# Optimization experiments

Hardware: AMD Instinct MI355X
Metric: run time of the kernel (lower is better)

Reference implementation:

```python
import jax, jax.numpy as jnp
import numpy as np

EPS = 1e-6
DECAY = 0.99
COMMIT = 0.25           # CONFIG['commitment_cost']
GRAPH_BIAS_SCALE = 0.8  # CONFIG['graph_bias_scale']
CONTEXT_INFLUENCE = 0.5 # CONFIG['context_influence']

N, LATENT, K = 16384, 512, 8192


def setup_inputs() -> dict:
    key = jax.random.key(0)
    ks = jax.random.split(key, 9)
    z_real = jax.random.normal(ks[0], (N, LATENT), jnp.float32)
    z_imag = jax.random.normal(ks[1], (N, LATENT), jnp.float32)
    ctx_real = jax.random.normal(ks[2], (N, LATENT), jnp.float32)
    ctx_imag = jax.random.normal(ks[3], (N, LATENT), jnp.float32)
    prev_symbol_idx = jax.random.randint(ks[4], (N,), 0, K, jnp.int32)
    codebook = jax.random.normal(ks[5], (K, 2 * LATENT), jnp.float32)
    adjacency = jax.random.normal(ks[6], (K, K), jnp.float32)
    # nn.Linear-style init scale for the context gate
    gate_w = jax.random.normal(ks[7], (K, 2 * LATENT), jnp.float32) / np.sqrt(2 * LATENT)
    gate_b = jax.random.normal(ks[8], (K,), jnp.float32) / np.sqrt(2 * LATENT)
    cluster_size = jnp.zeros((K,), jnp.float32)
    embed_avg = codebook.copy()
    return dict(z_real=z_real, z_imag=z_imag, ctx_real=ctx_real, ctx_imag=ctx_imag,
                prev_symbol_idx=prev_symbol_idx, codebook=codebook, adjacency=adjacency,
                gate_w=gate_w, gate_b=gate_b, cluster_size=cluster_size, embed_avg=embed_avg)


def reference(z_real, z_imag, ctx_real, ctx_imag, prev_symbol_idx, codebook,
              adjacency, gate_w, gate_b, cluster_size, embed_avg):
    n_symbols = codebook.shape[0]
    z_flat = jnp.concatenate([z_real, z_imag], axis=-1)          # [N, 2D]
    # squared euclidean distances to codebook: [N, K]
    d = (jnp.sum(z_flat ** 2, axis=1, keepdims=True)
         + jnp.sum(codebook ** 2, axis=1)
         - 2.0 * z_flat @ codebook.T)
    # graph-context bias
    static_prior = adjacency[prev_symbol_idx]                    # [N, K] row gather
    ctx_flat = jnp.concatenate([ctx_real, ctx_imag], axis=-1)    # [N, 2D]
    context_bias = ctx_flat @ gate_w.T + gate_b                  # [N, K]
    combined_prior = jax.nn.sigmoid(static_prior) * (1.0 + CONTEXT_INFLUENCE * jnp.tanh(context_bias))
    d = d - GRAPH_BIAS_SCALE * combined_prior

    min_indices = jnp.argmin(d, axis=1)                          # [N]
    z_q = codebook[min_indices]                                  # [N, 2D]

    # training-mode EMA codebook update (one-hot matmuls == segment sums)
    counts = jax.ops.segment_sum(jnp.ones_like(min_indices, jnp.float32), min_indices,
                                 num_segments=n_symbols)
    embed_sum = jax.ops.segment_sum(z_flat, min_indices, num_segments=n_symbols)
    new_cluster_size = cluster_size * DECAY + (1.0 - DECAY) * counts
    new_embed_avg = embed_avg * DECAY + (1.0 - DECAY) * embed_sum
    n_total = jnp.sum(new_cluster_size)
    cs = (new_cluster_size + EPS) / (n_total + n_symbols * EPS) * n_total
    new_codebook = new_embed_avg / cs[:, None]

    loss_vq = jnp.mean((z_q - jax.lax.stop_gradient(z_flat)) ** 2)
    loss_commit = jnp.mean((jax.lax.stop_gradient(z_q) - z_flat) ** 2)
    loss = loss_vq + COMMIT * loss_commit

    # straight-through estimator; complex output represented as concat(real, imag)
    z_q_st = z_flat + jax.lax.stop_gradient(z_q - z_flat)        # [N, 2D]
    return z_q_st, loss, min_indices, new_codebook, new_cluster_size, new_embed_avg
```

## Files before the change

### kernel.cpp

```cpp
#include <hip/hip_runtime.h>
#include <hip/hip_bf16.h>


#define NR 16384
#define DH 512
#define D2 1024
#define KS 8192
#define BK 128
#define BN 128
#define KC 64
#define KSPLIT 4
#define KRANGE (KS / KSPLIT)
#define NKT (KRANGE / BK)
#define TILE_B 16384

typedef __bf16 bf16x8 __attribute__((ext_vector_type(8)));
typedef float f32x4 __attribute__((ext_vector_type(4)));

#define WS_CNORM 0
#define WS_LOSS  32768
#define WS_NTOT  32776
#define WS_CAND  33024
#define WS_WIDX  (33024 + NR * 64 * 8)

typedef const __attribute__((address_space(1))) void* gas_t;
typedef __attribute__((address_space(3))) void* las_t;
__device__ __forceinline__ void gld16(const void* g, void* l) {
  __builtin_amdgcn_global_load_lds((gas_t)g, (las_t)l, 16, 0, 0);
}

#define LDSF(t, row, sl)                                                     \
  (*(const bf16x8*)((const char*)sbuf + (t)*TILE_B + (row)*128 +             \
                    (((sl) ^ ((row) & 7)) * 16)))

__global__ __launch_bounds__(256) void k_cvt(
    const float* __restrict__ zr, const float* __restrict__ zi,
    const float* __restrict__ cr, const float* __restrict__ ci,
    const float* __restrict__ cb, const float* __restrict__ gw,
    __hip_bfloat16* __restrict__ zb, __hip_bfloat16* __restrict__ xb,
    __hip_bfloat16* __restrict__ cbb, __hip_bfloat16* __restrict__ gwb) {
  const int flat = blockIdx.x * 256 + threadIdx.x;
  const int r_all = flat >> 7;
  const int g = flat & 127;
  const float* s0;
  const float* s1;
  __hip_bfloat16* dst;
  int r;
  if (r_all < NR)                { r = r_all;              s0 = zr; s1 = zi;      dst = zb;  }
  else if (r_all < 2 * NR)       { r = r_all - NR;         s0 = cr; s1 = ci;      dst = xb;  }
  else if (r_all < 2 * NR + KS)  { r = r_all - 2 * NR;     s0 = cb; s1 = nullptr; dst = cbb; }
  else                           { r = r_all - 2 * NR - KS; s0 = gw; s1 = nullptr; dst = gwb; }
  const int c = g * 8;
  const float* src;
  if (s1) src = (c < DH) ? s0 + (size_t)r * DH + c : s1 + (size_t)r * DH + (c - DH);
  else    src = s0 + (size_t)r * D2 + c;
  f32x4 f0 = *(const f32x4*)src;
  f32x4 f1 = *(const f32x4*)(src + 4);
  bf16x8 h;
  h[0] = (__bf16)f0.x; h[1] = (__bf16)f0.y; h[2] = (__bf16)f0.z; h[3] = (__bf16)f0.w;
  h[4] = (__bf16)f1.x; h[5] = (__bf16)f1.y; h[6] = (__bf16)f1.z; h[7] = (__bf16)f1.w;
  const int chunk = g >> 3, sl = g & 7;
  const int rr = r & 127, rb = r >> 7;
  const int slS = sl ^ (rr & 7);
  const size_t off = ((size_t)(rb * 16 + chunk) * 128 + rr) * 64 + slS * 8;
  *(bf16x8*)(dst + off) = h;
}

__global__ __launch_bounds__(64) void k_cnorm(const float* __restrict__ cb,
                                              float* __restrict__ cnorm) {
  int k = blockIdx.x, lane = threadIdx.x;
  const float* row = cb + (size_t)k * D2;
  float acc = 0.f;
#pragma unroll
  for (int j = 0; j < 4; ++j) {
    f32x4 v = *(const f32x4*)(row + j * 256 + lane * 4);
    acc += v.x * v.x + v.y * v.y + v.z * v.z + v.w * v.w;
  }
#pragma unroll
  for (int off = 32; off; off >>= 1) acc += __shfl_xor(acc, off);
  if (lane == 0) cnorm[k] = acc;
}

__global__ __launch_bounds__(256, 2) void k_phase1(
    const int* __restrict__ prev,
    const __hip_bfloat16* __restrict__ zb, const __hip_bfloat16* __restrict__ xb,
    const __hip_bfloat16* __restrict__ cbb, const __hip_bfloat16* __restrict__ gwb,
    const float* __restrict__ adj, const float* __restrict__ gb,
    const float* __restrict__ cnorm, int2* __restrict__ cand) {
  __shared__ unsigned short sbuf[4 * BK * KC];

  const int tid = threadIdx.x;
  const int lane = tid & 63;
  const int wid = tid >> 6;
  const int wavek = wid >> 1;
  const int waven = wid & 1;
  const int r16 = lane & 15;
  const int quad = lane >> 4;
  const int nb = blockIdx.x;
  const int n0 = nb * BN;
  const int bk = blockIdx.y;

  int nout[4];
  const float* arow[4];
#pragma unroll
  for (int nf = 0; nf < 4; ++nf) {
    nout[nf] = n0 + waven * 64 + nf * 16 + r16;
    arow[nf] = adj + (size_t)prev[nout[nf]] * KS;
  }

  float v0[4], v1[4];
  int i0[4], i1[4];
#pragma unroll
  for (int nf = 0; nf < 4; ++nf) { v0[nf] = 3.4e38f; v1[nf] = 3.4e38f; i0[nf] = 0; i1[nf] = 0; }

  for (int kt = 0; kt < NKT; ++kt) {
    const int ktg = bk * NKT + kt;
    const int k0 = ktg * BK;
    f32x4 accS[4][4], accX[4][4];
#pragma unroll
    for (int a = 0; a < 4; ++a)
#pragma unroll
      for (int b = 0; b < 4; ++b) {
        accS[a][b] = (f32x4){0.f, 0.f, 0.f, 0.f};
        accX[a][b] = (f32x4){0.f, 0.f, 0.f, 0.f};
      }

    for (int c = 0; c < D2 / KC; ++c) {
      const char* tb0 = (const char*)zb  + ((size_t)nb * 16 + c) * TILE_B;
      const char* tb1 = (const char*)xb  + ((size_t)nb * 16 + c) * TILE_B;
      const char* tb2 = (const char*)cbb + ((size_t)ktg * 16 + c) * TILE_B;
      const char* tb3 = (const char*)gwb + ((size_t)ktg * 16 + c) * TILE_B;
#pragma unroll
      for (int i = 0; i < 4; ++i) {
        const int o = (wid * 4 + i) * 1024;
        const int so = o + lane * 16;
        gld16(tb0 + so, (char*)sbuf + 0 * TILE_B + o);
        gld16(tb1 + so, (char*)sbuf + 1 * TILE_B + o);
        gld16(tb2 + so, (char*)sbuf + 2 * TILE_B + o);
        gld16(tb3 + so, (char*)sbuf + 3 * TILE_B + o);
      }
      __syncthreads();

#pragma unroll
      for (int s = 0; s < 2; ++s) {
        const int sl = s * 4 + quad;
        {
          bf16x8 a[4], b[4];
#pragma unroll
          for (int kf = 0; kf < 4; ++kf) a[kf] = LDSF(2, wavek * 64 + kf * 16 + r16, sl);
#pragma unroll
          for (int nf = 0; nf < 4; ++nf) b[nf] = LDSF(0, waven * 64 + nf * 16 + r16, sl);
#pragma unroll
          for (int kf = 0; kf < 4; ++kf)
#pragma unroll
            for (int nf = 0; nf < 4; ++nf)
              accS[kf][nf] =
                  __builtin_amdgcn_mfma_f32_16x16x32_bf16(a[kf], b[nf], accS[kf][nf], 0, 0, 0);
        }
        {
          bf16x8 a[4], b[4];
#pragma unroll
          for (int kf = 0; kf < 4; ++kf) a[kf] = LDSF(3, wavek * 64 + kf * 16 + r16, sl);
#pragma unroll
          for (int nf = 0; nf < 4; ++nf) b[nf] = LDSF(1, waven * 64 + nf * 16 + r16, sl);
#pragma unroll
          for (int kf = 0; kf < 4; ++kf)
#pragma unroll
            for (int nf = 0; nf < 4; ++nf)
              accX[kf][nf] =
                  __builtin_amdgcn_mfma_f32_16x16x32_bf16(a[kf], b[nf], accX[kf][nf], 0, 0, 0);
        }
      }
      __syncthreads();
    }

#pragma unroll
    for (int kf = 0; kf < 4; ++kf) {
      const int kb = k0 + wavek * 64 + kf * 16 + quad * 4;
      const f32x4 cn = *(const f32x4*)(cnorm + kb);
      const f32x4 g4 = *(const f32x4*)(gb + kb);
#pragma unroll
      for (int nf = 0; nf < 4; ++nf) {
        const f32x4 a4 = *(const f32x4*)(arow[nf] + kb);
#pragma unroll
        for (int r = 0; r < 4; ++r) {
          float s = accS[kf][nf][r];
          float x = accX[kf][nf][r] + g4[r];
          float sig = __fdividef(1.f, 1.f + __expf(-a4[r]));
          float e2 = __expf(2.f * x);
          float th = 1.f - __fdividef(2.f, e2 + 1.f);
          float sc = cn[r] - 2.f * s - 0.8f * sig * (1.f + 0.5f * th);
          int kk = kb + r;
          if (sc < v1[nf]) {
            if (sc < v0[nf]) {
              v1[nf] = v0[nf]; i1[nf] = i0[nf];
              v0[nf] = sc;     i0[nf] = kk;
            } else {
              v1[nf] = sc; i1[nf] = kk;
            }
          }
        }
      }
    }
  }

#pragma unroll
  for (int nf = 0; nf < 4; ++nf) {
    const int n = nout[nf];
    const int slot = ((bk * 2 + wavek) * 4 + quad) * 2;
    int2* p = cand + (size_t)n * 64 + slot;
    p[0] = make_int2(__float_as_int(v0[nf]), i0[nf]);
    p[1] = make_int2(__float_as_int(v1[nf]), i1[nf]);
  }
}

__global__ __launch_bounds__(256) void k_rescore(
    const float* __restrict__ zr, const float* __restrict__ zi,
    const float* __restrict__ cr, const float* __restrict__ ci,
    const int* __restrict__ prev, const float* __restrict__ cb,
    const float* __restrict__ adj, const float* __restrict__ gw,
    const float* __restrict__ gb, const int2* __restrict__ cand,
    int* __restrict__ widx, float* __restrict__ out_idx) {
  const int n = blockIdx.x * 4 + (threadIdx.x >> 6);
  const int lane = threadIdx.x & 63;

  f32x4 zv[4], xv[4];
#pragma unroll
  for (int j = 0; j < 4; ++j) {
    const int col = j * 256 + lane * 4;
    zv[j] = (col < DH) ? *(const f32x4*)(zr + (size_t)n * DH + col)
                       : *(const f32x4*)(zi + (size_t)n * DH + col - DH);
    xv[j] = (col < DH) ? *(const f32x4*)(cr + (size_t)n * DH + col)
                       : *(const f32x4*)(ci + (size_t)n * DH + col - DH);
  }

  int2 e = cand[(size_t)n * 64 + lane];
  float asc = __int_as_float(e.x);
  int aid = e.y;
  float m = asc;
#pragma unroll
  for (int off = 32; off; off >>= 1) m = fminf(m, __shfl_xor(m, off));
  unsigned long long mask = __ballot(asc <= m + 1.5f);

  const float* arow = adj + (size_t)prev[n] * KS;
  float best = 3.4e38f;
  int bid = 1 << 30;
  while (mask) {
    const int b = __ffsll((unsigned long long)mask) - 1;
    mask &= mask - 1;
    const int cidx = __shfl(aid, b);
    const float* crow = cb + (size_t)cidx * D2;
    const float* grow = gw + (size_t)cidx * D2;
    float sd = 0.f, xd = 0.f, cn = 0.f;
#pragma unroll
    for (int j = 0; j < 4; ++j) {
      f32x4 c4 = *(const f32x4*)(crow + j * 256 + lane * 4);
      f32x4 g4 = *(const f32x4*)(grow + j * 256 + lane * 4);
      sd += zv[j].x * c4.x + zv[j].y * c4.y + zv[j].z * c4.z + zv[j].w * c4.w;
      cn += c4.x * c4.x + c4.y * c4.y + c4.z * c4.z + c4.w * c4.w;
      xd += xv[j].x * g4.x + xv[j].y * g4.y + xv[j].z * g4.z + xv[j].w * g4.w;
    }
#pragma unroll
    for (int off = 32; off; off >>= 1) {
      sd += __shfl_xor(sd, off);
      cn += __shfl_xor(cn, off);
      xd += __shfl_xor(xd, off);
    }
    float xb2 = xd + gb[cidx];
    float sig = 1.f / (1.f + expf(-arow[cidx]));
    float th = tanhf(xb2);
    float sc = cn - 2.f * sd - 0.8f * sig * (1.f + 0.5f * th);
    if (sc < best || (sc == best && cidx < bid)) { best = sc; bid = cidx; }
  }
  if (lane == 0) { widx[n] = bid; out_idx[n] = (float)bid; }
}

__global__ __launch_bounds__(256) void k_gather(
    const float* __restrict__ zr, const float* __restrict__ zi,
    const float* __restrict__ cb, const int* __restrict__ widx,
    float* __restrict__ out0, float* __restrict__ esum, float* __restrict__ cnt,
    double* __restrict__ loss) {
  __shared__ float red[4];
  const int n = blockIdx.x, tid = threadIdx.x;
  const int w = widx[n];
  const int e = tid * 4;
  f32x4 zv = (e < DH) ? *(const f32x4*)(zr + (size_t)n * DH + e)
                      : *(const f32x4*)(zi + (size_t)n * DH + e - DH);
  f32x4 cq = *(const f32x4*)(cb + (size_t)w * D2 + e);
  f32x4 d, o;
  d.x = cq.x - zv.x; d.y = cq.y - zv.y; d.z = cq.z - zv.z; d.w = cq.w - zv.w;
  o.x = zv.x + d.x;  o.y = zv.y + d.y;  o.z = zv.z + d.z;  o.w = zv.w + d.w;
  *(f32x4*)(out0 + (size_t)n * D2 + e) = o;
  atomicAdd(esum + (size_t)w * D2 + e + 0, zv.x);
  atomicAdd(esum + (size_t)w * D2 + e + 1, zv.y);
  atomicAdd(esum + (size_t)w * D2 + e + 2, zv.z);
  atomicAdd(esum + (size_t)w * D2 + e + 3, zv.w);
  float lp = d.x * d.x + d.y * d.y + d.z * d.z + d.w * d.w;
#pragma unroll
  for (int off = 32; off; off >>= 1) lp += __shfl_xor(lp, off);
  if ((tid & 63) == 0) red[tid >> 6] = lp;
  __syncthreads();
  if (tid == 0) {
    atomicAdd(loss, (double)(red[0] + red[1] + red[2] + red[3]));
    atomicAdd(cnt + w, 1.0f);
  }
}

__global__ __launch_bounds__(256) void k_cs(const float* __restrict__ cs_in,
                                            float* __restrict__ o4,
                                            float* __restrict__ ntot,
                                            const double* __restrict__ loss,
                                            float* __restrict__ o1) {
  __shared__ float red[4];
  const int k = blockIdx.x * 256 + threadIdx.x;
  const float c = o4[k];
  const float ncs = cs_in[k] * 0.99f + 0.01f * c;
  o4[k] = ncs;
  float lp = ncs;
#pragma unroll
  for (int off = 32; off; off >>= 1) lp += __shfl_xor(lp, off);
  if ((threadIdx.x & 63) == 0) red[threadIdx.x >> 6] = lp;
  __syncthreads();
  if (threadIdx.x == 0) atomicAdd(ntot, red[0] + red[1] + red[2] + red[3]);
  if (blockIdx.x == 0 && threadIdx.x == 0)
    o1[0] = (float)(1.25 * loss[0] / 16777216.0);
}

__global__ __launch_bounds__(256) void k_final(const float* __restrict__ eavg,
                                               const float* __restrict__ o4,
                                               const float* __restrict__ ntotp,
                                               float* __restrict__ o3,
                                               float* __restrict__ o5) {
  const int k = blockIdx.x, tid = threadIdx.x;
  const float ntot = *ntotp;
  const float ncs = o4[k];
  const float csd = (ncs + 1e-6f) / (ntot + 0.008192f) * ntot;
#pragma unroll
  for (int j = 0; j < 4; ++j) {
    const int e = tid + j * 256;
    const size_t idx = (size_t)k * D2 + e;
    const float es = o5[idx];
    const float nea = eavg[idx] * 0.99f + 0.01f * es;
    o5[idx] = nea;
    o3[idx] = nea / csd;
  }
}

extern "C" void kernel_launch(void* const* d_in, const int* in_sizes, int n_in,
                              void* d_out, int out_size, void* d_ws, size_t ws_size,
                              hipStream_t stream) {
  const float* zr = (const float*)d_in[0];
  const float* zi = (const float*)d_in[1];
  const float* cr = (const float*)d_in[2];
  const float* ci = (const float*)d_in[3];
  const int* pv = (const int*)d_in[4];
  const float* cb = (const float*)d_in[5];
  const float* adj = (const float*)d_in[6];
  const float* gw = (const float*)d_in[7];
  const float* gb = (const float*)d_in[8];
  const float* cs = (const float*)d_in[9];
  const float* ea = (const float*)d_in[10];

  float* out = (float*)d_out;
  float* o0 = out;
  float* o1 = out + (size_t)NR * D2;
  float* o2 = o1 + 1;
  float* o3 = o2 + NR;
  float* o4 = o3 + (size_t)KS * D2;
  float* o5 = o4 + KS;

  char* ws = (char*)d_ws;
  float* cnorm = (float*)(ws + WS_CNORM);
  double* loss = (double*)(ws + WS_LOSS);
  float* ntot = (float*)(ws + WS_NTOT);
  int2* cand = (int2*)(ws + WS_CAND);
  int* widx = (int*)(ws + WS_WIDX);

  __hip_bfloat16* zb = (__hip_bfloat16*)o0;
  __hip_bfloat16* xb = zb + (size_t)NR * D2;
  uintptr_t cba = ((uintptr_t)o3 + 15) & ~(uintptr_t)15;
  __hip_bfloat16* cbb = (__hip_bfloat16*)cba;
  __hip_bfloat16* gwb = cbb + (size_t)KS * D2;

  k_cvt<<<(2 * NR + 2 * KS) * 128 / 256, 256, 0, stream>>>(zr, zi, cr, ci, cb, gw,
                                                           zb, xb, cbb, gwb);
  k_cnorm<<<KS, 64, 0, stream>>>(cb, cnorm);
  dim3 g1(NR / BN, KSPLIT);
  k_phase1<<<g1, 256, 0, stream>>>(pv, zb, xb, cbb, gwb, adj, gb, cnorm, cand);

  hipMemsetAsync(o4, 0, KS * sizeof(float), stream);
  hipMemsetAsync(o5, 0, (size_t)KS * D2 * sizeof(float), stream);
  hipMemsetAsync(ws + WS_LOSS, 0, 32, stream);

  k_rescore<<<NR / 4, 256, 0, stream>>>(zr, zi, cr, ci, pv, cb, adj, gw, gb, cand, widx, o2);
  k_gather<<<NR, 256, 0, stream>>>(zr, zi, cb, widx, o0, o5, o4, loss);
  k_cs<<<KS / 256, 256, 0, stream>>>(cs, o4, ntot, loss, o1);
  k_final<<<KS, 256, 0, stream>>>(ea, o4, ntot, o3, o5);
}
```

Measured before the change: 1.662 ms.

## Replace atomic scatter segment-sum with bucket sort and per-code gather reduction

Fuses the z_q output write and loss reduction into the rescore kernel. It also replaces the per-element float atomicAdd scatter into the embed-sum buffer with a counting sort: count, prefix scan, scatter into buckets, then one block per code sums its assigned rows. This removes the 16M float atomics and the large memset of the output buffer. The cost is several extra small launches, including a single-block scan. The per-code loop is also serial and could be unbalanced when many rows land on one code.

```diff
diff --git a/kernel.cpp b/kernel.cpp
--- a/kernel.cpp
+++ b/kernel.cpp
@@ -22,6 +22,10 @@
 #define WS_NTOT  32776
 #define WS_CAND  33024
 #define WS_WIDX  (33024 + NR * 64 * 8)
+#define OV_CNTI  WS_CAND
+#define OV_OFF   (WS_CAND + 32768)
+#define OV_POS   (WS_CAND + 65536)
+#define OV_BKT   (WS_CAND + 131072)
 
 typedef const __attribute__((address_space(1))) void* gas_t;
 typedef __attribute__((address_space(3))) void* las_t;
@@ -220,7 +224,8 @@
     const int* __restrict__ prev, const float* __restrict__ cb,
     const float* __restrict__ adj, const float* __restrict__ gw,
     const float* __restrict__ gb, const int2* __restrict__ cand,
-    int* __restrict__ widx, float* __restrict__ out_idx) {
+    int* __restrict__ widx, float* __restrict__ out_idx,
+    float* __restrict__ out0, double* __restrict__ loss) {
   const int n = blockIdx.x * 4 + (threadIdx.x >> 6);
   const int lane = threadIdx.x & 63;
 
@@ -272,49 +277,88 @@
     float sc = cn - 2.f * sd - 0.8f * sig * (1.f + 0.5f * th);
     if (sc < best || (sc == best && cidx < bid)) { best = sc; bid = cidx; }
   }
-  if (lane == 0) { widx[n] = bid; out_idx[n] = (float)bid; }
-}
-
-__global__ __launch_bounds__(256) void k_gather(
+  const float* crow = cb + (size_t)bid * D2;
+  float lp = 0.f;
+#pragma unroll
+  for (int j = 0; j < 4; ++j) {
+    const int col = j * 256 + lane * 4;
+    f32x4 cq = *(const f32x4*)(crow + col);
+    f32x4 d, o;
+    d.x = cq.x - zv[j].x; d.y = cq.y - zv[j].y; d.z = cq.z - zv[j].z; d.w = cq.w - zv[j].w;
+    o.x = zv[j].x + d.x;  o.y = zv[j].y + d.y;  o.z = zv[j].z + d.z;  o.w = zv[j].w + d.w;
+    *(f32x4*)(out0 + (size_t)n * D2 + col) = o;
+    lp += d.x * d.x + d.y * d.y + d.z * d.z + d.w * d.w;
+  }
+#pragma unroll
+  for (int off = 32; off; off >>= 1) lp += __shfl_xor(lp, off);
+  if (lane == 0) {
+    widx[n] = bid;
+    out_idx[n] = (float)bid;
+    atomicAdd(loss, (double)lp);
+  }
+}
+
+__global__ __launch_bounds__(256) void k_count(const int* __restrict__ widx,
+                                               int* __restrict__ cnti,
+                                               int* __restrict__ pos) {
+  const int n = blockIdx.x * 256 + threadIdx.x;
+  pos[n] = atomicAdd(&cnti[widx[n]], 1);
+}
+
+__global__ __launch_bounds__(256) void k_scan(const int* __restrict__ cnti,
+                                              int* __restrict__ off) {
+  __shared__ int part[256];
+  const int t = threadIdx.x;
+  int v[32];
+  int s = 0;
+#pragma unroll
+  for (int i = 0; i < 32; ++i) { v[i] = s; s += cnti[t * 32 + i]; }
+  part[t] = s;
+  __syncthreads();
+  if (t == 0) {
+    int run = 0;
+    for (int i = 0; i < 256; ++i) { int tmp = part[i]; part[i] = run; run += tmp; }
+  }
+  __syncthreads();
+  const int base = part[t];
+#pragma unroll
+  for (int i = 0; i < 32; ++i) off[t * 32 + i] = base + v[i];
+}
+
+__global__ __launch_bounds__(256) void k_scatter(const int* __restrict__ widx,
+                                                 const int* __restrict__ pos,
+                                                 const int* __restrict__ off,
+                                                 int* __restrict__ bucket) {
+  const int n = blockIdx.x * 256 + threadIdx.x;
+  bucket[off[widx[n]] + pos[n]] = n;
+}
+
+__global__ __launch_bounds__(256) void k_segsum(
     const float* __restrict__ zr, const float* __restrict__ zi,
-    const float* __restrict__ cb, const int* __restrict__ widx,
-    float* __restrict__ out0, float* __restrict__ esum, float* __restrict__ cnt,
-    double* __restrict__ loss) {
-  __shared__ float red[4];
-  const int n = blockIdx.x, tid = threadIdx.x;
-  const int w = widx[n];
+    const int* __restrict__ cnti, const int* __restrict__ off,
+    const int* __restrict__ bucket, float* __restrict__ esum) {
+  const int k = blockIdx.x, tid = threadIdx.x;
+  const int c = cnti[k], o = off[k];
   const int e = tid * 4;
-  f32x4 zv = (e < DH) ? *(const f32x4*)(zr + (size_t)n * DH + e)
-                      : *(const f32x4*)(zi + (size_t)n * DH + e - DH);
-  f32x4 cq = *(const f32x4*)(cb + (size_t)w * D2 + e);
-  f32x4 d, o;
-  d.x = cq.x - zv.x; d.y = cq.y - zv.y; d.z = cq.z - zv.z; d.w = cq.w - zv.w;
-  o.x = zv.x + d.x;  o.y = zv.y + d.y;  o.z = zv.z + d.z;  o.w = zv.w + d.w;
-  *(f32x4*)(out0 + (size_t)n * D2 + e) = o;
-  atomicAdd(esum + (size_t)w * D2 + e + 0, zv.x);
-  atomicAdd(esum + (size_t)w * D2 + e + 1, zv.y);
-  atomicAdd(esum + (size_t)w * D2 + e + 2, zv.z);
-  atomicAdd(esum + (size_t)w * D2 + e + 3, zv.w);
-  float lp = d.x * d.x + d.y * d.y + d.z * d.z + d.w * d.w;
-#pragma unroll
-  for (int off = 32; off; off >>= 1) lp += __shfl_xor(lp, off);
-  if ((tid & 63) == 0) red[tid >> 6] = lp;
-  __syncthreads();
-  if (tid == 0) {
-    atomicAdd(loss, (double)(red[0] + red[1] + red[2] + red[3]));
-    atomicAdd(cnt + w, 1.0f);
-  }
+  const float* src = (e < DH) ? zr + e : zi + (e - DH);
+  f32x4 acc = (f32x4){0.f, 0.f, 0.f, 0.f};
+  for (int i = 0; i < c; ++i) {
+    const int n = bucket[o + i];
+    f32x4 v = *(const f32x4*)(src + (size_t)n * DH);
+    acc.x += v.x; acc.y += v.y; acc.z += v.z; acc.w += v.w;
+  }
+  *(f32x4*)(esum + (size_t)k * D2 + e) = acc;
 }
 
 __global__ __launch_bounds__(256) void k_cs(const float* __restrict__ cs_in,
+                                            const int* __restrict__ cnti,
                                             float* __restrict__ o4,
                                             float* __restrict__ ntot,
                                             const double* __restrict__ loss,
                                             float* __restrict__ o1) {
   __shared__ float red[4];
   const int k = blockIdx.x * 256 + threadIdx.x;
-  const float c = o4[k];
-  const float ncs = cs_in[k] * 0.99f + 0.01f * c;
+  const float ncs = cs_in[k] * 0.99f + 0.01f * (float)cnti[k];
   o4[k] = ncs;
   float lp = ncs;
 #pragma unroll
@@ -375,6 +419,10 @@
   float* ntot = (float*)(ws + WS_NTOT);
   int2* cand = (int2*)(ws + WS_CAND);
   int* widx = (int*)(ws + WS_WIDX);
+  int* cnti = (int*)(ws + OV_CNTI);
+  int* offp = (int*)(ws + OV_OFF);
+  int* pos  = (int*)(ws + OV_POS);
+  int* bkt  = (int*)(ws + OV_BKT);
 
   __hip_bfloat16* zb = (__hip_bfloat16*)o0;
   __hip_bfloat16* xb = zb + (size_t)NR * D2;
@@ -388,12 +436,15 @@
   dim3 g1(NR / BN, KSPLIT);
   k_phase1<<<g1, 256, 0, stream>>>(pv, zb, xb, cbb, gwb, adj, gb, cnorm, cand);
 
-  hipMemsetAsync(o4, 0, KS * sizeof(float), stream);
-  hipMemsetAsync(o5, 0, (size_t)KS * D2 * sizeof(float), stream);
   hipMemsetAsync(ws + WS_LOSS, 0, 32, stream);
-
-  k_rescore<<<NR / 4, 256, 0, stream>>>(zr, zi, cr, ci, pv, cb, adj, gw, gb, cand, widx, o2);
-  k_gather<<<NR, 256, 0, stream>>>(zr, zi, cb, widx, o0, o5, o4, loss);
-  k_cs<<<KS / 256, 256, 0, stream>>>(cs, o4, ntot, loss, o1);
+  k_rescore<<<NR / 4, 256, 0, stream>>>(zr, zi, cr, ci, pv, cb, adj, gw, gb,
+                                        cand, widx, o2, o0, loss);
+
+  hipMemsetAsync(cnti, 0, KS * sizeof(int), stream);
+  k_count<<<NR / 256, 256, 0, stream>>>(widx, cnti, pos);
+  k_scan<<<1, 256, 0, stream>>>(cnti, offp);
+  k_scatter<<<NR / 256, 256, 0, stream>>>(widx, pos, offp, bkt);
+  k_segsum<<<KS, 256, 0, stream>>>(zr, zi, cnti, offp, bkt, o5);
+  k_cs<<<KS / 256, 256, 0, stream>>>(cs, cnti, o4, ntot, loss, o1);
   k_final<<<KS, 256, 0, stream>>>(ea, o4, ntot, o3, o5);
 }
```

New measurement: 1.598 ms. -3.9%, faster.
